# Optimization experiments

Measured on AMD Instinct MI355X. Metric: run time of the kernel, lower is better.

The kernel has to match this reference:

```python
import jax, jax.numpy as jnp
import numpy as np

# Device/group constants for group_idx = 0 (from the source)
V_REF = 0.25
G_MIN = 1.0 / 983.3
G_MAX = 1.0 / 281.3
N_AVG = 2.132
N_STD = 0.095

P, N_IN, N_OUT = 1024, 784, 128


def setup_inputs() -> dict:
    key = jax.random.key(0)
    k1, k2, k3, k4, k5, k6 = jax.random.split(key, 6)
    x = jax.random.uniform(k1, (P, N_IN), dtype=jnp.float32)  # normalized pixel-like inputs in [0,1)
    stdv = 1.0 / np.sqrt(N_IN)
    w_pos = 0.5 + stdv * jax.random.normal(k2, (N_IN, N_OUT), dtype=jnp.float32)
    w_neg = 0.5 + stdv * jax.random.normal(k3, (N_IN, N_OUT), dtype=jnp.float32)
    b_pos = 0.5 * jnp.ones((N_OUT,), dtype=jnp.float32)
    b_neg = 0.5 * jnp.ones((N_OUT,), dtype=jnp.float32)
    # per-device nonlinearity parameter n ~ N(n_avg, n_std), crossbar shape (m, 2*n_out)
    n_param = N_AVG + N_STD * jax.random.normal(k4, (N_IN + 1, 2 * N_OUT), dtype=jnp.float32)
    return {"x": x, "w_pos": w_pos, "w_neg": w_neg, "b_pos": b_pos, "b_neg": b_neg, "n_param": n_param}


def reference(x, w_pos, w_neg, b_pos, b_neg, n_param):
    # --- build combined (weights+bias row), pos/neg column-interleaved crossbar params ---
    cw_pos = jnp.concatenate([w_pos, b_pos[None, :]], axis=0)  # (m, n_out), m = n_in+1
    cw_neg = jnp.concatenate([w_neg, b_neg[None, :]], axis=0)  # (m, n_out)
    m = cw_pos.shape[0]
    weights = jnp.stack([cw_pos, cw_neg], axis=-1).reshape(m, -1)  # (m, 2*n_out), interleaved

    max_weight = jnp.max(jnp.abs(weights))
    # w_params_to_G: linear map of nonnegative weight params onto [G_min, G_max]
    G = G_MIN + (G_MAX - G_MIN) * weights / max_weight  # (m, 2n)

    # x_to_V with appended ones column (bias word line)
    k_V = 2.0 * V_REF
    ones = jnp.ones((x.shape[0], 1), dtype=x.dtype)
    inputs = jnp.concatenate([x, ones], axis=1)  # (p, m)
    V = k_V * inputs  # (p, m)

    # nonlinear IV: I(V) = sign(V) * G*V_ref * n ** log2(|V|/V_ref)
    exponent = jnp.log2(jnp.maximum(jnp.abs(V), 1e-12) / V_REF)  # (p, m)
    I_ind = jnp.sign(V)[:, :, None] * (V_REF * G)[None, :, :] * n_param[None, :, :] ** exponent[:, :, None]  # (p, m, 2n)
    I = jnp.sum(I_ind, axis=1)  # bit-line currents, (p, 2n)

    # I_to_y: differential pos-neg columns, undo conductance/voltage scaling
    I_total = I[:, 0::2] - I[:, 1::2]  # (p, n_out)
    y = I_total * (max_weight / (k_V * (G_MAX - G_MIN)))
    return y
```

## Files before the change

kernel.cpp:

```cpp
#include <hip/hip_runtime.h>
#include <hip/hip_bf16.h>

#define P_ROWS   1024
#define N_IN     784
#define N_OUT    128
#define M_ROWS   785
#define M_PAD    816
#define OUT_ELEMS (P_ROWS * N_OUT)

#define RATIO_F  ((float)((1.0/983.3) / ((1.0/281.3) - (1.0/983.3))))
#define L_AVG_F  1.0922076f
#define LN2_F    0.6931472f

#define NCH      24
#define CHUNK    34
#define NB_MAIN  ((P_ROWS / 32) * NCH)

#define NB_MAX   32

#define PART_OFF 0
#define C_OFF    256

typedef _Float16 half2v __attribute__((ext_vector_type(2)));
typedef _Float16 half4v __attribute__((ext_vector_type(4)));

__device__ __forceinline__ float fdot2(half2v a, half2v b, float c) {
#if __has_builtin(__builtin_amdgcn_fdot2)
    return __builtin_amdgcn_fdot2(a, b, c, false);
#else
    return fmaf((float)a.x, (float)b.x, fmaf((float)a.y, (float)b.y, c));
#endif
}

__global__ __launch_bounds__(256) void max_reduce(
        const float* __restrict__ wp, const float* __restrict__ wn,
        const float* __restrict__ bp, const float* __restrict__ bn,
        float* __restrict__ partial) {
    const int b = blockIdx.x, t = threadIdx.x;
    const int nW4 = (N_IN * N_OUT) / 4;
    const float4* wp4 = (const float4*)wp;
    const float4* wn4 = (const float4*)wn;
    int gid = b * 256 + t;
    float v = 0.0f;
    if (gid < N_OUT / 4) {
        float4 a = ((const float4*)bp)[gid], c = ((const float4*)bn)[gid];
        v = fmaxf(fmaxf(fmaxf(fabsf(a.x), fabsf(a.y)), fmaxf(fabsf(a.z), fabsf(a.w))),
                  fmaxf(fmaxf(fabsf(c.x), fabsf(c.y)), fmaxf(fabsf(c.z), fabsf(c.w))));
    }
    for (int i = gid; i < nW4; i += NB_MAX * 256) {
        float4 a = wp4[i], c = wn4[i];
        v = fmaxf(v, fmaxf(fmaxf(fabsf(a.x), fabsf(a.y)), fmaxf(fabsf(a.z), fabsf(a.w))));
        v = fmaxf(v, fmaxf(fmaxf(fabsf(c.x), fabsf(c.y)), fmaxf(fabsf(c.z), fabsf(c.w))));
    }
    for (int off = 32; off > 0; off >>= 1)
        v = fmaxf(v, __shfl_down(v, off, 64));
    __shared__ float smax[4];
    if ((t & 63) == 0) smax[t >> 6] = v;
    __syncthreads();
    if (t == 0)
        partial[b] = fmaxf(fmaxf(smax[0], smax[1]), fmaxf(smax[2], smax[3]));
}

__global__ __launch_bounds__(256) void precompute_c(
        const float* __restrict__ wp, const float* __restrict__ wn,
        const float* __restrict__ bp, const float* __restrict__ bn,
        const float* __restrict__ np, const float* __restrict__ partial,
        half4v* __restrict__ C) {
    float mw = 0.0f;
    #pragma unroll
    for (int i = 0; i < NB_MAX; ++i) mw = fmaxf(mw, partial[i]);
    const float c0 = 0.5f * RATIO_F * mw;

    int idx = blockIdx.x * 256 + threadIdx.x;
    int m = idx >> 7, k = idx & 127;
    half4v c = {0.0f16, 0.0f16, 0.0f16, 0.0f16};
    if (m < M_ROWS) {
        float wpv = (m < N_IN) ? wp[m * N_OUT + k] : bp[k];
        float wnv = (m < N_IN) ? wn[m * N_OUT + k] : bn[k];
        float npv = np[m * (2 * N_OUT) + 2 * k];
        float nnv = np[m * (2 * N_OUT) + 2 * k + 1];
        float Dp = LN2_F * (__builtin_amdgcn_logf(npv) - L_AVG_F);
        float Dn = LN2_F * (__builtin_amdgcn_logf(nnv) - L_AVG_F);
        float Ap = c0 + 0.5f * wpv;
        float An = c0 + 0.5f * wnv;
        float ApD = Ap * Dp,   AnD = An * Dn;
        float ApD2 = ApD * Dp, AnD2 = AnD * Dn;
        float ApD3 = ApD2 * Dp, AnD3 = AnD2 * Dn;
        c.x = (_Float16)(Ap - An);
        c.y = (_Float16)(ApD - AnD);
        c.z = (_Float16)((ApD2 - AnD2) * 0.5f);
        c.w = (_Float16)((ApD3 - AnD3) * (1.0f / 6.0f));
    }
    C[idx] = c;
}

__global__ __launch_bounds__(256) void memristor_main(
        const float* __restrict__ x, const half4v* __restrict__ C,
        float* __restrict__ out) {
    const int bid = blockIdx.x;
    const int ch  = bid % NCH;
    const int pb  = bid / NCH;
    const int p0  = pb * 32;
    const int m0  = ch * CHUNK;
    const int t   = threadIdx.x;

    __shared__ half4v F_lds[32][CHUNK];
    for (int idx = t; idx < 32 * CHUNK; idx += 256) {
        const int r  = idx / CHUNK;
        const int mm = idx - r * CHUNK;
        const int m  = m0 + mm;
        float e;
        if (m < N_IN) {
            float xv = x[(size_t)(p0 + r) * N_IN + m];
            e = (xv > 0.0f) ? __builtin_amdgcn_logf(2.0f * xv) : -1.0e4f;
        } else {
            e = (m == N_IN) ? 1.0f : -1.0e4f;
        }
        float F0 = __builtin_amdgcn_exp2f(e * L_AVG_F);
        float F1 = F0 * e;
        float F2 = F1 * e;
        float F3 = F2 * e;
        half4v f = {(_Float16)F0, (_Float16)F1, (_Float16)F2, (_Float16)F3};
        F_lds[r][mm] = f;
    }
    __syncthreads();

    const int lane = t & 63;
    const int pg   = t >> 6;
    const int k    = lane;

    const half4v* __restrict__ Cp = C + (size_t)m0 * N_OUT + k;
    const half4v* __restrict__ Fb = &F_lds[pg * 8][0];

    float acc[16];
    #pragma unroll
    for (int i = 0; i < 16; ++i) acc[i] = 0.0f;

    for (int mm = 0; mm < CHUNK; ++mm) {
        half4v c0 = Cp[(size_t)mm * N_OUT];
        half4v c1 = Cp[(size_t)mm * N_OUT + 64];
        half2v c0a = {c0.x, c0.y}, c0b = {c0.z, c0.w};
        half2v c1a = {c1.x, c1.y}, c1b = {c1.z, c1.w};
        #pragma unroll
        for (int i = 0; i < 8; ++i) {
            half4v f = Fb[i * CHUNK + mm];
            half2v fa = {f.x, f.y}, fb = {f.z, f.w};
            acc[2 * i]     = fdot2(fa, c0a, fdot2(fb, c0b, acc[2 * i]));
            acc[2 * i + 1] = fdot2(fa, c1a, fdot2(fb, c1b, acc[2 * i + 1]));
        }
    }

    float* o = out + (size_t)(p0 + pg * 8) * N_OUT + k;
    #pragma unroll
    for (int i = 0; i < 8; ++i) {
        unsafeAtomicAdd(o + (size_t)i * N_OUT,      acc[2 * i]);
        unsafeAtomicAdd(o + (size_t)i * N_OUT + 64, acc[2 * i + 1]);
    }
}

extern "C" void kernel_launch(void* const* d_in, const int* in_sizes, int n_in,
                              void* d_out, int out_size, void* d_ws, size_t ws_size,
                              hipStream_t stream) {
    const float* x  = (const float*)d_in[0];
    const float* wp = (const float*)d_in[1];
    const float* wn = (const float*)d_in[2];
    const float* bp = (const float*)d_in[3];
    const float* bn = (const float*)d_in[4];
    const float* np = (const float*)d_in[5];
    float* out = (float*)d_out;

    float*  partial = (float*)((char*)d_ws + PART_OFF);
    half4v* C       = (half4v*)((char*)d_ws + C_OFF);

    hipMemsetAsync(out, 0, (size_t)OUT_ELEMS * sizeof(float), stream);
    max_reduce<<<NB_MAX, 256, 0, stream>>>(wp, wn, bp, bn, partial);
    precompute_c<<<(M_PAD * N_OUT) / 256, 256, 0, stream>>>(wp, wn, bp, bn, np, partial, C);
    memristor_main<<<NB_MAIN, 256, 0, stream>>>(x, C, out);
}
```

Before: 89.62 us.

## Use MFMA f16 matrix cores for the main contraction with deterministic split-K combine

Replaces the per-thread fdot2 accumulation with 16x16x32 f16 MFMA instructions. The precomputed coefficient tensor is reordered into an MFMA-friendly blocked layout, and the F features are stored in LDS in matching fragment order. Atomic adds and the output memset are replaced by writing per-chunk partial sums to workspace, followed by a separate combine kernel that reduces the 12 chunks. This adds a fourth launch and extra partial-buffer traffic in return for much higher matrix throughput.

Result: faster. 78.58 us (-12.3%).

```diff
diff --git a/kernel.cpp b/kernel.cpp
--- a/kernel.cpp
+++ b/kernel.cpp
@@ -5,32 +5,28 @@
 #define N_IN     784
 #define N_OUT    128
 #define M_ROWS   785
-#define M_PAD    816
 #define OUT_ELEMS (P_ROWS * N_OUT)
 
 #define RATIO_F  ((float)((1.0/983.3) / ((1.0/281.3) - (1.0/983.3))))
 #define L_AVG_F  1.0922076f
 #define LN2_F    0.6931472f
 
-#define NCH      24
-#define CHUNK    34
-#define NB_MAIN  ((P_ROWS / 32) * NCH)
+#define NCHK   12
+#define MCH    72
+#define KCH    (MCH * 4)
+#define NSTEP  (KCH / 32)
+#define M_TOT  (NCHK * MCH)
+#define NB_MAIN (64 * NCHK)
 
-#define NB_MAX   32
+#define NB_MAX 32
 
-#define PART_OFF 0
-#define C_OFF    256
+#define PART_MAX_OFF 0
+#define CR_OFF       256
+#define CR_BYTES     ((size_t)M_TOT * 4 * 128 * 2)
+#define PARTIAL_OFF  (CR_OFF + CR_BYTES)
 
-typedef _Float16 half2v __attribute__((ext_vector_type(2)));
-typedef _Float16 half4v __attribute__((ext_vector_type(4)));
-
-__device__ __forceinline__ float fdot2(half2v a, half2v b, float c) {
-#if __has_builtin(__builtin_amdgcn_fdot2)
-    return __builtin_amdgcn_fdot2(a, b, c, false);
-#else
-    return fmaf((float)a.x, (float)b.x, fmaf((float)a.y, (float)b.y, c));
-#endif
-}
+typedef _Float16 half8 __attribute__((ext_vector_type(8)));
+typedef float    f32x4 __attribute__((ext_vector_type(4)));
 
 __global__ __launch_bounds__(256) void max_reduce(
         const float* __restrict__ wp, const float* __restrict__ wn,
@@ -65,97 +61,114 @@
         const float* __restrict__ wp, const float* __restrict__ wn,
         const float* __restrict__ bp, const float* __restrict__ bn,
         const float* __restrict__ np, const float* __restrict__ partial,
-        half4v* __restrict__ C) {
+        _Float16* __restrict__ Cr) {
     float mw = 0.0f;
     #pragma unroll
     for (int i = 0; i < NB_MAX; ++i) mw = fmaxf(mw, partial[i]);
     const float c0 = 0.5f * RATIO_F * mw;
 
     int idx = blockIdx.x * 256 + threadIdx.x;
-    int m = idx >> 7, k = idx & 127;
-    half4v c = {0.0f16, 0.0f16, 0.0f16, 0.0f16};
+    int m = idx >> 7, n = idx & 127;
+    float C0 = 0.f, C1 = 0.f, C2 = 0.f, C3 = 0.f;
     if (m < M_ROWS) {
-        float wpv = (m < N_IN) ? wp[m * N_OUT + k] : bp[k];
-        float wnv = (m < N_IN) ? wn[m * N_OUT + k] : bn[k];
-        float npv = np[m * (2 * N_OUT) + 2 * k];
-        float nnv = np[m * (2 * N_OUT) + 2 * k + 1];
+        float wpv = (m < N_IN) ? wp[m * N_OUT + n] : bp[n];
+        float wnv = (m < N_IN) ? wn[m * N_OUT + n] : bn[n];
+        float npv = np[m * (2 * N_OUT) + 2 * n];
+        float nnv = np[m * (2 * N_OUT) + 2 * n + 1];
         float Dp = LN2_F * (__builtin_amdgcn_logf(npv) - L_AVG_F);
         float Dn = LN2_F * (__builtin_amdgcn_logf(nnv) - L_AVG_F);
         float Ap = c0 + 0.5f * wpv;
         float An = c0 + 0.5f * wnv;
-        float ApD = Ap * Dp,   AnD = An * Dn;
-        float ApD2 = ApD * Dp, AnD2 = AnD * Dn;
+        float ApD = Ap * Dp,    AnD = An * Dn;
+        float ApD2 = ApD * Dp,  AnD2 = AnD * Dn;
         float ApD3 = ApD2 * Dp, AnD3 = AnD2 * Dn;
-        c.x = (_Float16)(Ap - An);
-        c.y = (_Float16)(ApD - AnD);
-        c.z = (_Float16)((ApD2 - AnD2) * 0.5f);
-        c.w = (_Float16)((ApD3 - AnD3) * (1.0f / 6.0f));
+        C0 = Ap - An;
+        C1 = ApD - AnD;
+        C2 = (ApD2 - AnD2) * 0.5f;
+        C3 = (ApD3 - AnD3) * (1.0f / 6.0f);
     }
-    C[idx] = c;
+    const int c  = m / MCH;
+    const int ml = m - c * MCH;
+    const int s  = ml >> 3;
+    const int q  = (ml >> 1) & 3;
+    const int h  = (ml & 1) * 4;
+    _Float16* dst = Cr + (((((size_t)c * NSTEP + s) * 4 + q) * 128 + n) * 8 + h);
+    dst[0] = (_Float16)C0;
+    dst[1] = (_Float16)C1;
+    dst[2] = (_Float16)C2;
+    dst[3] = (_Float16)C3;
 }
 
 __global__ __launch_bounds__(256) void memristor_main(
-        const float* __restrict__ x, const half4v* __restrict__ C,
-        float* __restrict__ out) {
+        const float* __restrict__ x, const _Float16* __restrict__ Cr,
+        float* __restrict__ part) {
     const int bid = blockIdx.x;
-    const int ch  = bid % NCH;
-    const int pb  = bid / NCH;
-    const int p0  = pb * 32;
-    const int m0  = ch * CHUNK;
+    const int ch  = bid % NCHK;
+    const int pb  = bid / NCHK;
+    const int p0  = pb * 16;
+    const int m0  = ch * MCH;
     const int t   = threadIdx.x;
 
-    __shared__ half4v F_lds[32][CHUNK];
-    for (int idx = t; idx < 32 * CHUNK; idx += 256) {
-        const int r  = idx / CHUNK;
-        const int mm = idx - r * CHUNK;
-        const int m  = m0 + mm;
+    __shared__ half8 F_lds[36 * 16];
+    for (int pm = t; pm < 16 * MCH; pm += 256) {
+        const int p  = pm / MCH;
+        const int ml = pm - p * MCH;
+        const int m  = m0 + ml;
         float e;
         if (m < N_IN) {
-            float xv = x[(size_t)(p0 + r) * N_IN + m];
+            float xv = x[(size_t)(p0 + p) * N_IN + m];
             e = (xv > 0.0f) ? __builtin_amdgcn_logf(2.0f * xv) : -1.0e4f;
         } else {
             e = (m == N_IN) ? 1.0f : -1.0e4f;
         }
         float F0 = __builtin_amdgcn_exp2f(e * L_AVG_F);
-        float F1 = F0 * e;
-        float F2 = F1 * e;
-        float F3 = F2 * e;
-        half4v f = {(_Float16)F0, (_Float16)F1, (_Float16)F2, (_Float16)F3};
-        F_lds[r][mm] = f;
+        float F1 = F0 * e, F2 = F1 * e, F3 = F2 * e;
+        _Float16* dst = (_Float16*)&F_lds[(ml >> 1) * 16 + p] + (ml & 1) * 4;
+        dst[0] = (_Float16)F0;
+        dst[1] = (_Float16)F1;
+        dst[2] = (_Float16)F2;
+        dst[3] = (_Float16)F3;
     }
     __syncthreads();
 
     const int lane = t & 63;
-    const int pg   = t >> 6;
-    const int k    = lane;
+    const int w    = t >> 6;
+    const int quad = lane >> 4;
+    const int col  = lane & 15;
+    const int n0   = w * 32;
 
-    const half4v* __restrict__ Cp = C + (size_t)m0 * N_OUT + k;
-    const half4v* __restrict__ Fb = &F_lds[pg * 8][0];
+    const _Float16* __restrict__ Bb = Cr + (size_t)ch * (NSTEP * 4 * 128 * 8);
 
-    float acc[16];
-    #pragma unroll
-    for (int i = 0; i < 16; ++i) acc[i] = 0.0f;
-
-    for (int mm = 0; mm < CHUNK; ++mm) {
-        half4v c0 = Cp[(size_t)mm * N_OUT];
-        half4v c1 = Cp[(size_t)mm * N_OUT + 64];
-        half2v c0a = {c0.x, c0.y}, c0b = {c0.z, c0.w};
-        half2v c1a = {c1.x, c1.y}, c1b = {c1.z, c1.w};
-        #pragma unroll
-        for (int i = 0; i < 8; ++i) {
-            half4v f = Fb[i * CHUNK + mm];
-            half2v fa = {f.x, f.y}, fb = {f.z, f.w};
-            acc[2 * i]     = fdot2(fa, c0a, fdot2(fb, c0b, acc[2 * i]));
-            acc[2 * i + 1] = fdot2(fa, c1a, fdot2(fb, c1b, acc[2 * i + 1]));
-        }
+    f32x4 acc0 = {0.f, 0.f, 0.f, 0.f};
+    f32x4 acc1 = {0.f, 0.f, 0.f, 0.f};
+    #pragma unroll 3
+    for (int s = 0; s < NSTEP; ++s) {
+        half8 a  = F_lds[(s * 4 + quad) * 16 + col];
+        half8 b0 = *(const half8*)(Bb + (((s * 4 + quad) * 128) + n0 + col) * 8);
+        half8 b1 = *(const half8*)(Bb + (((s * 4 + quad) * 128) + n0 + 16 + col) * 8);
+        acc0 = __builtin_amdgcn_mfma_f32_16x16x32_f16(a, b0, acc0, 0, 0, 0);
+        acc1 = __builtin_amdgcn_mfma_f32_16x16x32_f16(a, b1, acc1, 0, 0, 0);
     }
 
-    float* o = out + (size_t)(p0 + pg * 8) * N_OUT + k;
+    float* pbase = part + (size_t)ch * OUT_ELEMS + (size_t)(p0 + quad * 4) * N_OUT;
     #pragma unroll
-    for (int i = 0; i < 8; ++i) {
-        unsafeAtomicAdd(o + (size_t)i * N_OUT,      acc[2 * i]);
-        unsafeAtomicAdd(o + (size_t)i * N_OUT + 64, acc[2 * i + 1]);
+    for (int r = 0; r < 4; ++r) {
+        pbase[(size_t)r * N_OUT + n0 + col]      = acc0[r];
+        pbase[(size_t)r * N_OUT + n0 + 16 + col] = acc1[r];
     }
+}
+
+__global__ __launch_bounds__(256) void combine(
+        const float* __restrict__ part, float* __restrict__ out) {
+    const int i = blockIdx.x * 256 + threadIdx.x;
+    const float4* p4 = (const float4*)part;
+    float4 s = p4[i];
+    #pragma unroll
+    for (int c = 1; c < NCHK; ++c) {
+        float4 v = p4[(size_t)c * (OUT_ELEMS / 4) + i];
+        s.x += v.x; s.y += v.y; s.z += v.z; s.w += v.w;
+    }
+    ((float4*)out)[i] = s;
 }
 
 extern "C" void kernel_launch(void* const* d_in, const int* in_sizes, int n_in,
@@ -169,11 +182,12 @@
     const float* np = (const float*)d_in[5];
     float* out = (float*)d_out;
 
-    float*  partial = (float*)((char*)d_ws + PART_OFF);
-    half4v* C       = (half4v*)((char*)d_ws + C_OFF);
+    float*     partial = (float*)((char*)d_ws + PART_MAX_OFF);
+    _Float16*  Cr      = (_Float16*)((char*)d_ws + CR_OFF);
+    float*     part    = (float*)((char*)d_ws + PARTIAL_OFF);
 
-    hipMemsetAsync(out, 0, (size_t)OUT_ELEMS * sizeof(float), stream);
     max_reduce<<<NB_MAX, 256, 0, stream>>>(wp, wn, bp, bn, partial);
-    precompute_c<<<(M_PAD * N_OUT) / 256, 256, 0, stream>>>(wp, wn, bp, bn, np, partial, C);
-    memristor_main<<<NB_MAIN, 256, 0, stream>>>(x, C, out);
+    precompute_c<<<(M_TOT * 128) / 256, 256, 0, stream>>>(wp, wn, bp, bn, np, partial, Cr);
+    memristor_main<<<NB_MAIN, 256, 0, stream>>>(x, Cr, part);
+    combine<<<OUT_ELEMS / 4 / 256, 256, 0, stream>>>(part, out);
 }
```
